# Kernel optimization log

Measured on AMD Instinct MI355X. Metric: run time of the kernel, lower is better.

Reference implementation:

```python
import jax, jax.numpy as jnp
import numpy as np
from jax import lax

N, D, H, E = 8192, 1024, 4096, 8


def setup_inputs() -> dict:
    key = jax.random.key(0)
    ks = jax.random.split(key, 7)
    s = 0.02
    return {
        "x": jax.random.normal(ks[0], (N, D), dtype=jnp.float32),
        "Wr": jax.random.normal(ks[1], (E, D), dtype=jnp.float32) * s,
        "br": jnp.zeros((E,), dtype=jnp.float32),
        "Wup": jax.random.normal(ks[2], (E, H, D), dtype=jnp.float32) * s,
        "bup": jnp.zeros((E, H), dtype=jnp.float32),
        "Wdown": jax.random.normal(ks[3], (E, D, H), dtype=jnp.float32) * s,
        "bdown": jnp.zeros((E, D), dtype=jnp.float32),
    }


def reference(x, Wr, br, Wup, bup, Wdown, bdown):
    # Router: softmax over logits; only argmax is used (softmax is monotone,
    # argmax of softmax == argmax of logits).
    logits = x @ Wr.T + br            # [N, E]
    scores = jax.nn.softmax(logits, axis=-1)
    top1 = jnp.argmax(scores, axis=-1)  # [N] int

    out0 = jnp.zeros_like(x)

    def body(out, ew):
        i, Wu, bu, Wd, bd = ew
        h = jax.nn.silu(x @ Wu.T + bu)   # [N, H]
        y = h @ Wd.T + bd                # [N, D]
        out = jnp.where((top1 == i)[:, None], y, out)
        return out, None

    idx = jnp.arange(Wup.shape[0])
    out, _ = lax.scan(body, out0, (idx, Wup, bup, Wdown, bdown))
    return out
```

## Files before the change

### kernel.cpp

```cpp
#include <hip/hip_runtime.h>

#define NT 8192
#define DD 1024
#define HH 4096
#define EE 8

typedef __attribute__((ext_vector_type(8))) short short8;
typedef __attribute__((ext_vector_type(4))) float f32x4;

__device__ __forceinline__ unsigned short f2bf(float f) {
    unsigned int u = __float_as_uint(f);
    u += 0x7FFFu + ((u >> 16) & 1u);
    return (unsigned short)(u >> 16);
}

__device__ __forceinline__ void gload_lds16(const void* g, void* l) {
    __builtin_amdgcn_global_load_lds(
        (const __attribute__((address_space(1))) unsigned int*)g,
        (__attribute__((address_space(3))) unsigned int*)l, 16, 0, 0);
}

__global__ __launch_bounds__(256) void cvtw_kernel(const float* __restrict__ a,
                                                   const float* __restrict__ b,
                                                   unsigned short* __restrict__ da,
                                                   unsigned short* __restrict__ db) {
    const size_t half = (size_t)EE * HH * DD;
    size_t i = ((size_t)blockIdx.x * 256 + threadIdx.x) * 8;
    const float* s; unsigned short* d;
    if (i < half) { s = a + i; d = da + i; }
    else          { s = b + (i - half); d = db + (i - half); }
    float4 v0 = ((const float4*)s)[0];
    float4 v1 = ((const float4*)s)[1];
    ushort4 o0, o1;
    o0.x = f2bf(v0.x); o0.y = f2bf(v0.y); o0.z = f2bf(v0.z); o0.w = f2bf(v0.w);
    o1.x = f2bf(v1.x); o1.y = f2bf(v1.y); o1.z = f2bf(v1.z); o1.w = f2bf(v1.w);
    ((ushort4*)d)[0] = o0;
    ((ushort4*)d)[1] = o1;
}

__global__ __launch_bounds__(256) void router_kernel(const float* __restrict__ x,
                                                     const float* __restrict__ Wr,
                                                     const float* __restrict__ br,
                                                     int* __restrict__ counts,
                                                     int* __restrict__ tlist) {
    __shared__ float sW[EE * DD];
    const int t = threadIdx.x;
    for (int i = t; i < EE * DD / 4; i += 256)
        ((float4*)sW)[i] = ((const float4*)Wr)[i];
    __syncthreads();
    const int lane = t & 63;
    const int wv = t >> 6;
    const int token = blockIdx.x * 4 + wv;
    const float* xr = x + (size_t)token * DD;
    float acc[EE];
#pragma unroll
    for (int e = 0; e < EE; e++) acc[e] = 0.f;
    for (int k = lane; k < DD; k += 64) {
        float xv = xr[k];
#pragma unroll
        for (int e = 0; e < EE; e++) acc[e] += xv * sW[e * DD + k];
    }
#pragma unroll
    for (int off = 32; off > 0; off >>= 1) {
#pragma unroll
        for (int e = 0; e < EE; e++) acc[e] += __shfl_xor(acc[e], off);
    }
    if (lane == 0) {
        int best = 0;
        float bv = acc[0] + br[0];
#pragma unroll
        for (int e = 1; e < EE; e++) {
            float v = acc[e] + br[e];
            if (v > bv) { bv = v; best = e; }
        }
        int pos = atomicAdd(&counts[best], 1);
        tlist[best * NT + pos] = token;
    }
}

__global__ __launch_bounds__(256) void gather_kernel(const float* __restrict__ x,
                                                     const int* __restrict__ tlist,
                                                     const int* __restrict__ counts,
                                                     unsigned short* __restrict__ xg) {
    const int row = blockIdx.x * 4 + (threadIdx.x >> 6);
    const int lane = threadIdx.x & 63;
    int off[EE];
    int s = 0;
#pragma unroll
    for (int k = 0; k < EE; k++) { off[k] = s; s += counts[k]; }
    int e = 0;
#pragma unroll
    for (int k = 1; k < EE; k++)
        if (row >= off[k]) e = k;
    const int token = tlist[e * NT + row - off[e]];
    const float4* src = (const float4*)(x + (size_t)token * DD);
    ushort4* dst = (ushort4*)(xg + (size_t)row * DD);
#pragma unroll
    for (int it = 0; it < 4; it++) {
        float4 v = src[it * 64 + lane];
        ushort4 o;
        o.x = f2bf(v.x); o.y = f2bf(v.y); o.z = f2bf(v.z); o.w = f2bf(v.w);
        dst[it * 64 + lane] = o;
    }
}


__global__ __launch_bounds__(256) void up_gemm(const unsigned short* __restrict__ xg,
                                               const unsigned short* __restrict__ Wub,
                                               const float* __restrict__ bup,
                                               const int* __restrict__ counts,
                                               unsigned short* __restrict__ hbuf) {
    const int e = blockIdx.z;
    int off_e = 0, cnt;
    {
        int s = 0;
#pragma unroll
        for (int k = 0; k < EE; k++) { if (k == e) off_e = s; s += counts[k]; }
        cnt = counts[e];
    }
    const int m0 = blockIdx.y * 128;
    if (m0 >= cnt) return;
    const int n0 = blockIdx.x * 128;
    const int t = threadIdx.x;

    __shared__ unsigned short sA[2][128 * 32];
    __shared__ unsigned short sB[2][128 * 32];

    const int r0 = t >> 2;
    const int kc = (t & 3) ^ ((r0 >> 1) & 3);
    const int c1 = cnt - 1;
    int ra = m0 + r0;      if (ra > c1) ra = c1;
    int rb = m0 + 64 + r0; if (rb > c1) rb = c1;
    const unsigned short* gA0 = xg + (size_t)(off_e + ra) * DD + kc * 8;
    const unsigned short* gA1 = xg + (size_t)(off_e + rb) * DD + kc * 8;
    const unsigned short* gB0 = Wub + ((size_t)e * HH + n0 + r0) * DD + kc * 8;
    const unsigned short* gB1 = Wub + ((size_t)e * HH + n0 + 64 + r0) * DD + kc * 8;

    const int lane = t & 63;
    const int wm = ((t >> 6) & 1) * 64;
    const int wn = (t >> 7) * 64;
    const int mrow = lane & 15;
    const int kq = lane >> 4;
    const int slot = (kq ^ ((mrow >> 1) & 3)) * 8;

    f32x4 acc[4][4];
#pragma unroll
    for (int i = 0; i < 4; i++)
#pragma unroll
        for (int j = 0; j < 4; j++)
            acc[i][j] = (f32x4){0.f, 0.f, 0.f, 0.f};

    auto STAGE = [&](int buf, int kt) {
        gload_lds16(gA0 + kt, &sA[buf][t * 8]);
        gload_lds16(gA1 + kt, &sA[buf][(t + 256) * 8]);
        gload_lds16(gB0 + kt, &sB[buf][t * 8]);
        gload_lds16(gB1 + kt, &sB[buf][(t + 256) * 8]);
    };

    STAGE(0, 0);
    int cur = 0;
    for (int kt = 0; kt < DD; kt += 32) {
        __syncthreads();
        if (kt + 32 < DD) STAGE(cur ^ 1, kt + 32);
        short8 a[4], b[4];
#pragma unroll
        for (int i = 0; i < 4; i++) {
            a[i] = *(const short8*)(&sA[cur][(wm + i * 16 + mrow) * 32 + slot]);
            b[i] = *(const short8*)(&sB[cur][(wn + i * 16 + mrow) * 32 + slot]);
        }
#pragma unroll
        for (int i = 0; i < 4; i++)
#pragma unroll
            for (int j = 0; j < 4; j++)
                acc[i][j] = __builtin_amdgcn_mfma_f32_16x16x32_bf16(a[i], b[j], acc[i][j], 0, 0, 0);
        cur ^= 1;
    }

    float bias[4];
#pragma unroll
    for (int j = 0; j < 4; j++) bias[j] = bup[e * HH + n0 + wn + j * 16 + mrow];
#pragma unroll
    for (int i = 0; i < 4; i++) {
#pragma unroll
        for (int r = 0; r < 4; r++) {
            int m = m0 + wm + i * 16 + kq * 4 + r;
            if (m < cnt) {
                unsigned short* hrow = hbuf + (size_t)(off_e + m) * HH + n0 + wn + mrow;
#pragma unroll
                for (int j = 0; j < 4; j++) {
                    float v = acc[i][j][r] + bias[j];
                    v = v / (1.f + __expf(-v));
                    hrow[j * 16] = f2bf(v);
                }
            }
        }
    }
}

__global__ __launch_bounds__(256) void down_gemm(const unsigned short* __restrict__ hbuf,
                                                 const unsigned short* __restrict__ Wdb,
                                                 const float* __restrict__ bdown,
                                                 const int* __restrict__ counts,
                                                 const int* __restrict__ tlist,
                                                 float* __restrict__ out) {
    const int e = blockIdx.z;
    int off_e = 0, cnt;
    {
        int s = 0;
#pragma unroll
        for (int k = 0; k < EE; k++) { if (k == e) off_e = s; s += counts[k]; }
        cnt = counts[e];
    }
    const int m0 = blockIdx.y * 128;
    if (m0 >= cnt) return;
    const int n0 = blockIdx.x * 128;
    const int t = threadIdx.x;

    __shared__ unsigned short sA[2][128 * 64];
    __shared__ unsigned short sB[2][128 * 64];

    const int r = t >> 3;
    const int c = t & 7;
    const int c1 = cnt - 1;
    const unsigned short* gA[4];
    const unsigned short* gB[4];
#pragma unroll
    for (int i = 0; i < 4; i++) {
        int row = r + 32 * i;
        int sc = c ^ (row & 7);
        int ra = m0 + row; if (ra > c1) ra = c1;
        gA[i] = hbuf + (size_t)(off_e + ra) * HH + sc * 8;
        gB[i] = Wdb + ((size_t)e * DD + n0 + row) * HH + sc * 8;
    }

    const int lane = t & 63;
    const int wm = ((t >> 6) & 1) * 64;
    const int wn = (t >> 7) * 64;
    const int mrow = lane & 15;
    const int kq = lane >> 4;

    f32x4 acc[4][4];
#pragma unroll
    for (int i = 0; i < 4; i++)
#pragma unroll
        for (int j = 0; j < 4; j++)
            acc[i][j] = (f32x4){0.f, 0.f, 0.f, 0.f};

    auto STAGE = [&](int buf, int kt) {
#pragma unroll
        for (int i = 0; i < 4; i++)
            gload_lds16(gA[i] + kt, &sA[buf][(i * 256 + t) * 8]);
#pragma unroll
        for (int i = 0; i < 4; i++)
            gload_lds16(gB[i] + kt, &sB[buf][(i * 256 + t) * 8]);
    };

    STAGE(0, 0);
    int cur = 0;
    for (int kt = 0; kt < HH; kt += 64) {
        __syncthreads();
        if (kt + 64 < HH) STAGE(cur ^ 1, kt + 64);
#pragma unroll
        for (int h = 0; h < 2; h++) {
            const int slot = (((h << 2) | kq) ^ (mrow & 7)) * 8;
            short8 a[4], b[4];
#pragma unroll
            for (int i = 0; i < 4; i++) {
                a[i] = *(const short8*)(&sA[cur][(wm + i * 16 + mrow) * 64 + slot]);
                b[i] = *(const short8*)(&sB[cur][(wn + i * 16 + mrow) * 64 + slot]);
            }
#pragma unroll
            for (int i = 0; i < 4; i++)
#pragma unroll
                for (int j = 0; j < 4; j++)
                    acc[i][j] = __builtin_amdgcn_mfma_f32_16x16x32_bf16(a[i], b[j], acc[i][j], 0, 0, 0);
        }
        cur ^= 1;
    }

    const int* tl = tlist + e * NT;
    float bias[4];
#pragma unroll
    for (int j = 0; j < 4; j++) bias[j] = bdown[e * DD + n0 + wn + j * 16 + mrow];
#pragma unroll
    for (int i = 0; i < 4; i++) {
#pragma unroll
        for (int r2 = 0; r2 < 4; r2++) {
            int m = m0 + wm + i * 16 + kq * 4 + r2;
            if (m < cnt) {
                int token = tl[m];
                float* orow = out + (size_t)token * DD + n0 + wn + mrow;
#pragma unroll
                for (int j = 0; j < 4; j++)
                    orow[j * 16] = acc[i][j][r2] + bias[j];
            }
        }
    }
}

extern "C" void kernel_launch(void* const* d_in, const int* in_sizes, int n_in,
                              void* d_out, int out_size, void* d_ws, size_t ws_size,
                              hipStream_t stream) {
    const float* x     = (const float*)d_in[0];
    const float* Wr    = (const float*)d_in[1];
    const float* br    = (const float*)d_in[2];
    const float* Wup   = (const float*)d_in[3];
    const float* bup   = (const float*)d_in[4];
    const float* Wdown = (const float*)d_in[5];
    const float* bdown = (const float*)d_in[6];
    float* out = (float*)d_out;

    char* w = (char*)d_ws;
    int* counts  = (int*)w;               w += 256;
    int* tlist   = (int*)w;               w += (size_t)EE * NT * 4;
    unsigned short* xg   = (unsigned short*)w;  w += (size_t)NT * DD * 2;
    unsigned short* hbuf = (unsigned short*)w;  w += (size_t)NT * HH * 2;
    unsigned short* Wub  = (unsigned short*)w;  w += (size_t)EE * HH * DD * 2;
    unsigned short* Wdb  = (unsigned short*)w;

    hipMemsetAsync(counts, 0, EE * sizeof(int), stream);

    cvtw_kernel<<<(2 * (size_t)EE * HH * DD) / 2048, 256, 0, stream>>>(Wup, Wdown, Wub, Wdb);
    router_kernel<<<NT / 4, 256, 0, stream>>>(x, Wr, br, counts, tlist);
    gather_kernel<<<NT / 4, 256, 0, stream>>>(x, tlist, counts, xg);

    dim3 gu(HH / 128, NT / 128, EE);
    up_gemm<<<gu, 256, 0, stream>>>(xg, Wub, bup, counts, hbuf);
    dim3 gd(DD / 128, NT / 128, EE);
    down_gemm<<<gd, 256, 0, stream>>>(hbuf, Wdb, bdown, counts, tlist, out);
}
```

Measured before the change: 724.3 us.

## Compact GEMM grids to flat expert-tile slots and shrink down-GEMM K tile

Replaces the 3D grid (n-tiles × 64 m-tiles × 8 experts) with a flat list of 72 slots decoded from the per-expert counts. This removes the many blocks that launched only to exit early. The down GEMM also moves from a 64-wide K tile to a 32-wide K tile, using the same swizzle as the up GEMM. That halves LDS use, which may raise occupancy, but doubles the number of barriers per K. The slot count of 72 assumes the summed ceil(count/128) never exceeds 72, which always holds for 8192 tokens over 8 experts.

```diff
diff --git a/kernel.cpp b/kernel.cpp
--- a/kernel.cpp
+++ b/kernel.cpp
@@ -105,21 +105,33 @@
 }
 
 
+#define SLOTS 72
+
+struct SlotDec { int e, off_e, cnt, m0, ok; };
+
+__device__ __forceinline__ SlotDec decode_slot(const int* __restrict__ counts, int slot) {
+    SlotDec d; d.ok = 0; d.e = 0; d.off_e = 0; d.cnt = 0; d.m0 = 0;
+    int s = 0, csum = 0;
+#pragma unroll
+    for (int k = 0; k < EE; k++) {
+        int ck = counts[k];
+        int mb = (ck + 127) >> 7;
+        if (!d.ok && slot < csum + mb) {
+            d.ok = 1; d.e = k; d.off_e = s; d.cnt = ck; d.m0 = (slot - csum) * 128;
+        }
+        s += ck; csum += mb;
+    }
+    return d;
+}
+
 __global__ __launch_bounds__(256) void up_gemm(const unsigned short* __restrict__ xg,
                                                const unsigned short* __restrict__ Wub,
                                                const float* __restrict__ bup,
                                                const int* __restrict__ counts,
                                                unsigned short* __restrict__ hbuf) {
-    const int e = blockIdx.z;
-    int off_e = 0, cnt;
-    {
-        int s = 0;
-#pragma unroll
-        for (int k = 0; k < EE; k++) { if (k == e) off_e = s; s += counts[k]; }
-        cnt = counts[e];
-    }
-    const int m0 = blockIdx.y * 128;
-    if (m0 >= cnt) return;
+    SlotDec sd = decode_slot(counts, blockIdx.y);
+    if (!sd.ok) return;
+    const int e = sd.e, off_e = sd.off_e, cnt = sd.cnt, m0 = sd.m0;
     const int n0 = blockIdx.x * 128;
     const int t = threadIdx.x;
 
@@ -203,41 +215,31 @@
                                                  const int* __restrict__ counts,
                                                  const int* __restrict__ tlist,
                                                  float* __restrict__ out) {
-    const int e = blockIdx.z;
-    int off_e = 0, cnt;
-    {
-        int s = 0;
-#pragma unroll
-        for (int k = 0; k < EE; k++) { if (k == e) off_e = s; s += counts[k]; }
-        cnt = counts[e];
-    }
-    const int m0 = blockIdx.y * 128;
-    if (m0 >= cnt) return;
+    SlotDec sd = decode_slot(counts, blockIdx.y);
+    if (!sd.ok) return;
+    const int e = sd.e, off_e = sd.off_e, cnt = sd.cnt, m0 = sd.m0;
     const int n0 = blockIdx.x * 128;
     const int t = threadIdx.x;
 
-    __shared__ unsigned short sA[2][128 * 64];
-    __shared__ unsigned short sB[2][128 * 64];
-
-    const int r = t >> 3;
-    const int c = t & 7;
+    __shared__ unsigned short sA[2][128 * 32];
+    __shared__ unsigned short sB[2][128 * 32];
+
+    const int r0 = t >> 2;
+    const int kc = (t & 3) ^ ((r0 >> 1) & 3);
     const int c1 = cnt - 1;
-    const unsigned short* gA[4];
-    const unsigned short* gB[4];
-#pragma unroll
-    for (int i = 0; i < 4; i++) {
-        int row = r + 32 * i;
-        int sc = c ^ (row & 7);
-        int ra = m0 + row; if (ra > c1) ra = c1;
-        gA[i] = hbuf + (size_t)(off_e + ra) * HH + sc * 8;
-        gB[i] = Wdb + ((size_t)e * DD + n0 + row) * HH + sc * 8;
-    }
+    int ra = m0 + r0;      if (ra > c1) ra = c1;
+    int rb = m0 + 64 + r0; if (rb > c1) rb = c1;
+    const unsigned short* gA0 = hbuf + (size_t)(off_e + ra) * HH + kc * 8;
+    const unsigned short* gA1 = hbuf + (size_t)(off_e + rb) * HH + kc * 8;
+    const unsigned short* gB0 = Wdb + ((size_t)e * DD + n0 + r0) * HH + kc * 8;
+    const unsigned short* gB1 = Wdb + ((size_t)e * DD + n0 + 64 + r0) * HH + kc * 8;
 
     const int lane = t & 63;
     const int wm = ((t >> 6) & 1) * 64;
     const int wn = (t >> 7) * 64;
     const int mrow = lane & 15;
     const int kq = lane >> 4;
+    const int slot = (kq ^ ((mrow >> 1) & 3)) * 8;
 
     f32x4 acc[4][4];
 #pragma unroll
@@ -247,34 +249,28 @@
             acc[i][j] = (f32x4){0.f, 0.f, 0.f, 0.f};
 
     auto STAGE = [&](int buf, int kt) {
-#pragma unroll
-        for (int i = 0; i < 4; i++)
-            gload_lds16(gA[i] + kt, &sA[buf][(i * 256 + t) * 8]);
-#pragma unroll
-        for (int i = 0; i < 4; i++)
-            gload_lds16(gB[i] + kt, &sB[buf][(i * 256 + t) * 8]);
+        gload_lds16(gA0 + kt, &sA[buf][t * 8]);
+        gload_lds16(gA1 + kt, &sA[buf][(t + 256) * 8]);
+        gload_lds16(gB0 + kt, &sB[buf][t * 8]);
+        gload_lds16(gB1 + kt, &sB[buf][(t + 256) * 8]);
     };
 
     STAGE(0, 0);
     int cur = 0;
-    for (int kt = 0; kt < HH; kt += 64) {
+    for (int kt = 0; kt < HH; kt += 32) {
         __syncthreads();
-        if (kt + 64 < HH) STAGE(cur ^ 1, kt + 64);
-#pragma unroll
-        for (int h = 0; h < 2; h++) {
-            const int slot = (((h << 2) | kq) ^ (mrow & 7)) * 8;
-            short8 a[4], b[4];
-#pragma unroll
-            for (int i = 0; i < 4; i++) {
-                a[i] = *(const short8*)(&sA[cur][(wm + i * 16 + mrow) * 64 + slot]);
-                b[i] = *(const short8*)(&sB[cur][(wn + i * 16 + mrow) * 64 + slot]);
-            }
-#pragma unroll
-            for (int i = 0; i < 4; i++)
-#pragma unroll
-                for (int j = 0; j < 4; j++)
-                    acc[i][j] = __builtin_amdgcn_mfma_f32_16x16x32_bf16(a[i], b[j], acc[i][j], 0, 0, 0);
-        }
+        if (kt + 32 < HH) STAGE(cur ^ 1, kt + 32);
+        short8 a[4], b[4];
+#pragma unroll
+        for (int i = 0; i < 4; i++) {
+            a[i] = *(const short8*)(&sA[cur][(wm + i * 16 + mrow) * 32 + slot]);
+            b[i] = *(const short8*)(&sB[cur][(wn + i * 16 + mrow) * 32 + slot]);
+        }
+#pragma unroll
+        for (int i = 0; i < 4; i++)
+#pragma unroll
+            for (int j = 0; j < 4; j++)
+                acc[i][j] = __builtin_amdgcn_mfma_f32_16x16x32_bf16(a[i], b[j], acc[i][j], 0, 0, 0);
         cur ^= 1;
     }
 
@@ -285,14 +281,14 @@
 #pragma unroll
     for (int i = 0; i < 4; i++) {
 #pragma unroll
-        for (int r2 = 0; r2 < 4; r2++) {
-            int m = m0 + wm + i * 16 + kq * 4 + r2;
+        for (int r = 0; r < 4; r++) {
+            int m = m0 + wm + i * 16 + kq * 4 + r;
             if (m < cnt) {
                 int token = tl[m];
                 float* orow = out + (size_t)token * DD + n0 + wn + mrow;
 #pragma unroll
                 for (int j = 0; j < 4; j++)
-                    orow[j * 16] = acc[i][j][r2] + bias[j];
+                    orow[j * 16] = acc[i][j][r] + bias[j];
             }
         }
     }
@@ -324,8 +320,8 @@
     router_kernel<<<NT / 4, 256, 0, stream>>>(x, Wr, br, counts, tlist);
     gather_kernel<<<NT / 4, 256, 0, stream>>>(x, tlist, counts, xg);
 
-    dim3 gu(HH / 128, NT / 128, EE);
+    dim3 gu(HH / 128, SLOTS);
     up_gemm<<<gu, 256, 0, stream>>>(xg, Wub, bup, counts, hbuf);
-    dim3 gd(DD / 128, NT / 128, EE);
+    dim3 gd(DD / 128, SLOTS);
     down_gemm<<<gd, 256, 0, stream>>>(hbuf, Wdb, bdown, counts, tlist, out);
 }
```

New measurement: 691.9 us. -4.5%, faster.
